# Performance work log

Measured on AMD Instinct MI355X. Metric: run time of the kernel, lower is better.

Reference implementation:

```python
import jax, jax.numpy as jnp
import numpy as np

T, B, D, H = 2048, 2, 1024, 16
DPH = D // H
SCALE = DPH ** -0.5


def setup_inputs() -> dict:
    key = jax.random.key(0)
    ks = jax.random.split(key, 5)
    x = jax.random.normal(ks[0], (T, B, D), dtype=jnp.float32)
    Wk = jax.random.normal(ks[1], (D, D), dtype=jnp.float32) * 0.02
    Wv = jax.random.normal(ks[2], (D, D), dtype=jnp.float32) * 0.02
    Wq = jax.random.normal(ks[3], (D, D), dtype=jnp.float32) * 0.02
    Wo = jax.random.normal(ks[4], (D, D), dtype=jnp.float32) * 0.02
    # causal mask: True marks positions to hide (masked_fill semantics)
    mask = jnp.triu(jnp.ones((T, T), dtype=bool), k=1)
    return {"x": x, "Wk": Wk, "Wv": Wv, "Wq": Wq, "Wo": Wo, "mask": mask}


def _split_heads(y):
    # 't b (d h) -> b h t d' : d_per_head is the OUTER factor of the split
    t, b, _ = y.shape
    return y.reshape(t, b, DPH, H).transpose(1, 3, 0, 2)  # [b, h, t, d]


def reference(x, Wk, Wv, Wq, Wo, mask):
    # nn.Linear(bias=False): y = x @ W.T
    k = _split_heads(x @ Wk.T)
    v = _split_heads(x @ Wv.T)
    q = _split_heads(x @ Wq.T)
    scores = jnp.einsum('bhid,bhjd->bhij', q, k) * SCALE  # [b,h,t,t]
    scores = jnp.where(mask, -jnp.inf, scores)
    attn = jax.nn.softmax(scores, axis=-1)
    # dropout is identity in eval mode
    out = jnp.einsum('bhij,bhjd->bhid', attn, v)  # [b,h,t,d]
    # 'b h t d -> t b (h d)' : heads are the OUTER factor of the merge
    out = out.transpose(2, 0, 1, 3).reshape(x.shape[0], x.shape[1], D)
    return out @ Wo.T
```

## Files before the change

### kernel.cpp

```cpp
#include <hip/hip_runtime.h>

#define T_LEN   2048
#define BATCH   2
#define DMODEL  1024
#define NHEAD   16
#define DHEAD   64
#define MROWS   4096
#define KDIM    1024
#define NDIM    1024
#define ATT_SC2 (0.125f * 1.44269504088896f)

typedef unsigned short u16;
typedef unsigned int   u32;
typedef u16   u16x8 __attribute__((ext_vector_type(8)));
typedef u16   u16x4 __attribute__((ext_vector_type(4)));
typedef u32   u32x4 __attribute__((ext_vector_type(4)));
typedef __bf16 bf16x8 __attribute__((ext_vector_type(8)));
typedef float f32x4  __attribute__((ext_vector_type(4)));
typedef float f32x16 __attribute__((ext_vector_type(16)));

__device__ __forceinline__ u16 f2bf(float f) {
  u32 u = __builtin_bit_cast(u32, f);
  u += 0x7fffu + ((u >> 16) & 1u);
  return (u16)(u >> 16);
}

__device__ __forceinline__ u16 bfc(float f) {
  return __builtin_bit_cast(u16, (__bf16)f);
}

__device__ __forceinline__ f32x4 mfma16(u16x8 a, u16x8 b, f32x4 c) {
  return __builtin_amdgcn_mfma_f32_16x16x32_bf16(
      __builtin_bit_cast(bf16x8, a), __builtin_bit_cast(bf16x8, b), c, 0, 0, 0);
}

__device__ __forceinline__ f32x16 mfma32(u16x8 a, u16x8 b, f32x16 c) {
  return __builtin_amdgcn_mfma_f32_32x32x16_bf16(
      __builtin_bit_cast(bf16x8, a), __builtin_bit_cast(bf16x8, b), c, 0, 0, 0);
}

__device__ __forceinline__ f32x16 mfma32p(u32x4 a, u16x8 b, f32x16 c) {
  return __builtin_amdgcn_mfma_f32_32x32x16_bf16(
      __builtin_bit_cast(bf16x8, a), __builtin_bit_cast(bf16x8, b), c, 0, 0, 0);
}

__device__ __forceinline__ u32 cvtpk(float lo, float hi) {
  u32 r;
  asm("v_cvt_pk_bf16_f32 %0, %1, %2" : "=v"(r) : "v"(lo), "v"(hi));
  return r;
}

__device__ __forceinline__ void pswap(u32& a, u32& b) {
  asm volatile("v_permlane32_swap_b32 %0, %1" : "+v"(a), "+v"(b));
}

__device__ __forceinline__ void gload16(const u16* g, u16* l) {
  __builtin_amdgcn_global_load_lds((const __attribute__((address_space(1))) void*)g,
                                   (__attribute__((address_space(3))) void*)l,
                                   16, 0, 0);
}

#define XN 4194304u
__global__ __launch_bounds__(256) void cast_all(
    const float* __restrict__ x,  const float* __restrict__ wk,
    const float* __restrict__ wv, const float* __restrict__ wq,
    const float* __restrict__ wo, u16* __restrict__ ws) {
  size_t i = ((size_t)blockIdx.x * 256 + threadIdx.x) * 4;
  const float* src; size_t soff, doff; float sc = 1.0f;
  if (i < XN) {
    int m = (int)(i >> 10), d = (int)(i & 1023);
    int t = m >> 1, b = m & 1;
    src = x; soff = i;
    doff = ((size_t)(b * 2048 + t) << 10) + d;
  } else {
    size_t off = i - XN;
    int wi = (int)(off >> 20);
    off &= 1048575u;
    int u = (int)(off >> 10), c = (int)(off & 1023);
    src = (wi == 0) ? wk : (wi == 1) ? wv : (wi == 2) ? wq : wo;
    soff = off;
    if (wi == 3) {
      doff = XN + 3u * 1048576u + off;
    } else {
      int slot = (wi == 2) ? 0 : (wi == 0) ? 1 : 2;
      int up = (u & 15) * 64 + (u >> 4);
      doff = XN + (size_t)slot * 1048576u + ((size_t)up << 10) + c;
      if (wi == 2) sc = ATT_SC2;
    }
  }
  float4 v = *reinterpret_cast<const float4*>(src + soff);
  u16x4 o;
  o.s0 = f2bf(v.x * sc); o.s1 = f2bf(v.y * sc); o.s2 = f2bf(v.z * sc); o.s3 = f2bf(v.w * sc);
  *reinterpret_cast<u16x4*>(ws + doff) = o;
}

__global__ __launch_bounds__(256, 2) void gemm_qkv(
    const u16* __restrict__ xbm, const u16* __restrict__ Wqkv,
    u16* __restrict__ Qh, u16* __restrict__ Kh, u16* __restrict__ Vt) {
  __shared__ __align__(16) u16 As[256 * 64];
  __shared__ __align__(16) u16 Bs[128 * 64];

  const int tid = threadIdx.x;
  const int l  = tid & 63, w = tid >> 6;
  const int lr = l & 15,  lg = l >> 4;
  const int wm = w >> 1,  wn = w & 1;

  const int blk  = blockIdx.x;
  const int wgid = (blk & 7) * 48 + (blk >> 3);

  const u16 *A, *W;
  int m0, n0, isV;
  if (wgid < 256) {
    const int bx = wgid >> 4, by = wgid & 15;
    A = xbm; W = Wqkv; m0 = by * 256; n0 = bx * 128; isV = 0;
  } else {
    const int v = wgid - 256;
    const int vby = v >> 5, vbx = v & 31;
    A = Wqkv + (2048u << 10); W = xbm; m0 = vby * 256; n0 = vbx * 128; isV = 1;
  }

  f32x4 acc[8][4];
#pragma unroll
  for (int i = 0; i < 8; ++i)
#pragma unroll
    for (int j = 0; j < 4; ++j) acc[i][j] = (f32x4)(0.0f);

  for (int k0 = 0; k0 < KDIM; k0 += 64) {
#pragma unroll
    for (int i = 0; i < 8; ++i) {
      const int base = i * 256 + w * 64;
      const int p = base + l;
      const int r = p >> 3, c = p & 7;
      gload16(A + (size_t)(m0 + r) * KDIM + k0 + ((c ^ (r & 7)) << 3),
              As + (size_t)base * 8);
    }
#pragma unroll
    for (int i = 0; i < 4; ++i) {
      const int base = i * 256 + w * 64;
      const int p = base + l;
      const int r = p >> 3, c = p & 7;
      gload16(W + (size_t)(n0 + r) * KDIM + k0 + ((c ^ (r & 7)) << 3),
              Bs + (size_t)base * 8);
    }
    __syncthreads();

#pragma unroll
    for (int ks = 0; ks < 2; ++ks) {
      const int cr = ks * 4 + lg;
      u16x8 bf_[4];
#pragma unroll
      for (int ni = 0; ni < 4; ++ni) {
        const int rr = wn * 64 + ni * 16 + lr;
        bf_[ni] = *reinterpret_cast<const u16x8*>(Bs + rr * 64 + ((cr ^ (rr & 7)) << 3));
      }
      __builtin_amdgcn_s_setprio(1);
#pragma unroll
      for (int mi = 0; mi < 8; ++mi) {
        const int rr = wm * 128 + mi * 16 + lr;
        const u16x8 af = *reinterpret_cast<const u16x8*>(
            As + rr * 64 + ((cr ^ (rr & 7)) << 3));
#pragma unroll
        for (int ni = 0; ni < 4; ++ni)
          acc[mi][ni] = mfma16(af, bf_[ni], acc[mi][ni]);
      }
      __builtin_amdgcn_s_setprio(0);
    }
    __syncthreads();
  }

#pragma unroll
  for (int mi = 0; mi < 8; ++mi)
#pragma unroll
    for (int ni = 0; ni < 4; ++ni)
#pragma unroll
      for (int r = 0; r < 4; ++r) {
        const int row = m0 + wm * 128 + mi * 16 + lg * 4 + r;
        const int col = n0 + wn * 64 + ni * 16 + lr;
        const u16 v = bfc(acc[mi][ni][r]);
        if (!isV) {
          const int bb = row >> 11, t = row & 2047;
          const int c = col & 1023, hh = c >> 6, dp = c & 63;
          u16* d = (col < 1024) ? Qh : Kh;
          d[(((size_t)(bb * NHEAD + hh) << 11) + t) * 64 + dp] = v;
        } else {
          const int hh = row >> 6, dp = row & 63;
          const int bb = col >> 11, t = col & 2047;
          Vt[((((size_t)(bb * NHEAD + hh)) * 64 + dp) << 11) + t] = v;
        }
      }
}

__global__ __launch_bounds__(256) void gemm_o(
    const u16* __restrict__ A, const u16* __restrict__ W, float* __restrict__ out) {
  __shared__ __align__(16) u16 As[128 * 64];
  __shared__ __align__(16) u16 Bs[64 * 64];

  const int tid = threadIdx.x;
  const int l  = tid & 63, w = tid >> 6;
  const int lr = l & 15,  lg = l >> 4;
  const int wm = w >> 1,  wn = w & 1;

  const int blk  = blockIdx.x;
  const int wgid = (blk & 7) * 64 + (blk >> 3);
  const int bx = wgid >> 5, by = wgid & 31;
  const int m0 = by * 128;
  const int n0 = bx * 64;

  f32x4 acc[4][2];
#pragma unroll
  for (int i = 0; i < 4; ++i)
#pragma unroll
    for (int j = 0; j < 2; ++j) acc[i][j] = (f32x4)(0.0f);

  for (int k0 = 0; k0 < KDIM; k0 += 64) {
#pragma unroll
    for (int i = 0; i < 4; ++i) {
      const int base = i * 256 + w * 64;
      const int p = base + l;
      const int r = p >> 3, c = p & 7;
      gload16(A + (size_t)(m0 + r) * KDIM + k0 + ((c ^ (r & 7)) << 3),
              As + (size_t)base * 8);
    }
#pragma unroll
    for (int i = 0; i < 2; ++i) {
      const int base = i * 256 + w * 64;
      const int p = base + l;
      const int r = p >> 3, c = p & 7;
      gload16(W + (size_t)(n0 + r) * KDIM + k0 + ((c ^ (r & 7)) << 3),
              Bs + (size_t)base * 8);
    }
    __syncthreads();

#pragma unroll
    for (int ks = 0; ks < 2; ++ks) {
      const int cr = ks * 4 + lg;
      u16x8 bf_[2];
#pragma unroll
      for (int ni = 0; ni < 2; ++ni) {
        const int rr = wn * 32 + ni * 16 + lr;
        bf_[ni] = *reinterpret_cast<const u16x8*>(Bs + rr * 64 + ((cr ^ (rr & 7)) << 3));
      }
      __builtin_amdgcn_s_setprio(1);
#pragma unroll
      for (int mi = 0; mi < 4; ++mi) {
        const int rr = wm * 64 + mi * 16 + lr;
        const u16x8 af = *reinterpret_cast<const u16x8*>(
            As + rr * 64 + ((cr ^ (rr & 7)) << 3));
#pragma unroll
        for (int ni = 0; ni < 2; ++ni)
          acc[mi][ni] = mfma16(af, bf_[ni], acc[mi][ni]);
      }
      __builtin_amdgcn_s_setprio(0);
    }
    __syncthreads();
  }

#pragma unroll
  for (int mi = 0; mi < 4; ++mi)
#pragma unroll
    for (int ni = 0; ni < 2; ++ni)
#pragma unroll
      for (int r = 0; r < 4; ++r) {
        const int row = m0 + wm * 64 + mi * 16 + lg * 4 + r;
        const int col = n0 + wn * 32 + ni * 16 + lr;
        const int t = row & 2047, bb = row >> 11;
        out[((size_t)(t * 2 + bb) << 10) + col] = acc[mi][ni][r];
      }
}

__global__ __launch_bounds__(256, 2) void attn_fwd(
    const u16* __restrict__ Qh, const u16* __restrict__ Kh,
    const u16* __restrict__ Vt, u16* __restrict__ Aout) {
  __shared__ __align__(16) u16 smem[32768];

  const int tid = threadIdx.x;
  const int l = tid & 63, w = tid >> 6;
  const int l31 = l & 31, hi = l >> 5;
  const int wk = w & 1, wq = w >> 1;
  const int blk = blockIdx.x;
  const int bxx = (blk >> 3) & 15;
  const int bh  = ((blk >> 7) << 3) + (blk & 7);
  const int b = bh >> 4, h = bh & 15;

  const u16* kg = Kh + ((size_t)bh << 17);
  const u16* vg = Vt + ((size_t)bh << 17);

  float* redO = reinterpret_cast<float*>(smem);
  float* redS = redO + 4352;

  auto stage = [&](int buf, int kv0) {
    u16* kb = smem + buf * 8192;
    u16* vb = smem + 16384 + buf * 8192;
#pragma unroll
    for (int j = 0; j < 4; ++j) {
      const int base = (j * 4 + w) * 64;
      const int gg = base + l;
      const int rk = gg >> 3, ck = gg & 7;
      gload16(kg + (size_t)(kv0 + rk) * 64 + ((ck ^ (rk & 7)) << 3),
              kb + (size_t)base * 8);
      const int rv = gg >> 4, cv = gg & 15;
      gload16(vg + ((size_t)rv << 11) + kv0 + ((cv ^ (rv & 15)) << 3),
              vb + (size_t)base * 8);
    }
  };

  for (int ph = 0; ph < 2; ++ph) {
    const int qb = ph ? bxx : 31 - bxx;
    const int qbw = qb * 64 + wq * 32;
    const int q31 = qbw + l31;

    const u16* qptr = Qh + (((size_t)bh << 11) + q31) * 64 + hi * 8;
    u16x8 qf[4];
#pragma unroll
    for (int ks = 0; ks < 4; ++ks)
      qf[ks] = *reinterpret_cast<const u16x8*>(qptr + ks * 16);

    f32x16 acc0 = (f32x16)(0.0f), acc1 = (f32x16)(0.0f);
    float sumw = 0.0f;

    const int npair = (qb + 2) >> 1;
    stage(0, 0);
    __syncthreads();

    int cur = 0;
    for (int t = 0; t < npair; ++t) {
      const int kv0 = t * 128;
      const bool pf = (t + 1 < npair);
      if (pf) {
        stage(cur ^ 1, kv0 + 128);
        asm volatile("s_waitcnt vmcnt(8)" ::: "memory");
      } else {
        asm volatile("s_waitcnt vmcnt(0)" ::: "memory");
      }
      __builtin_amdgcn_sched_barrier(0);
      __builtin_amdgcn_s_barrier();

      const int kvw = kv0 + wk * 64;
      if (kvw <= qbw + 31) {
        const u16* kb = smem + cur * 8192;
        const u16* vb = smem + 16384 + cur * 8192;

#pragma unroll
        for (int tile = 0; tile < 2; ++tile) {
          const int tb = kvw + tile * 32;
          if (tb <= qbw + 31) {
            f32x16 s16 = (f32x16)(0.0f);
            __builtin_amdgcn_s_setprio(1);
#pragma unroll
            for (int ks = 0; ks < 4; ++ks) {
              const int row = wk * 64 + tile * 32 + l31;
              const u16x8 kf = *reinterpret_cast<const u16x8*>(
                  kb + row * 64 + (((2 * ks + hi) ^ (row & 7)) << 3));
              s16 = mfma32(kf, qf[ks], s16);
            }
            __builtin_amdgcn_s_setprio(0);

            const bool diag = (tb + 31 > qbw);
#pragma unroll
            for (int i = 0; i < 16; ++i) {
              float s = s16[i];
              if (diag) {
                const int kv = tb + (i & 3) + 8 * (i >> 2) + 4 * hi;
                if (kv > q31) s = -1e30f;
              }
              s16[i] = __builtin_amdgcn_exp2f(s - 8.0f);
            }
            float ts = 0.0f;
#pragma unroll
            for (int i = 0; i < 16; ++i) ts += s16[i];
            sumw += ts;

#pragma unroll
            for (int ks2 = 0; ks2 < 2; ++ks2) {
              const int pb = ks2 * 8;
              u32 a0 = cvtpk(s16[pb + 0], s16[pb + 1]);
              u32 b0 = cvtpk(s16[pb + 4], s16[pb + 5]);
              u32 a1 = cvtpk(s16[pb + 2], s16[pb + 3]);
              u32 b1 = cvtpk(s16[pb + 6], s16[pb + 7]);
              pswap(a0, b0);
              pswap(a1, b1);
              u32x4 pa;
              pa.x = a0; pa.y = a1; pa.z = b0; pa.w = b1;

              const int cc = wk * 8 + tile * 4 + ks2 * 2 + hi;
              __builtin_amdgcn_s_setprio(1);
              {
                const int dr0 = l31;
                const u16x8 vf0 = *reinterpret_cast<const u16x8*>(
                    vb + dr0 * 128 + ((cc ^ (dr0 & 15)) << 3));
                acc0 = mfma32p(pa, vf0, acc0);
                const int dr1 = 32 + l31;
                const u16x8 vf1 = *reinterpret_cast<const u16x8*>(
                    vb + dr1 * 128 + ((cc ^ (dr1 & 15)) << 3));
                acc1 = mfma32p(pa, vf1, acc1);
              }
              __builtin_amdgcn_s_setprio(0);
            }
          }
        }
      }

      asm volatile("s_waitcnt lgkmcnt(0)" ::: "memory");
      __builtin_amdgcn_sched_barrier(0);
      __builtin_amdgcn_s_barrier();
      cur ^= 1;
    }

    const float sfull = sumw + __shfl_xor(sumw, 32, 64);

    if (wk) {
      float* po = redO + wq * 2176;
#pragma unroll
      for (int i = 0; i < 16; ++i) {
        const int qr = (i & 3) + 8 * (i >> 2) + 4 * hi;
        po[qr * 68 + l31]      = acc0[i];
        po[qr * 68 + 32 + l31] = acc1[i];
      }
      if (l < 32) redS[wq * 32 + l] = sfull;
    }
    __syncthreads();

    if (!wk) {
      const float* po = redO + wq * 2176;
      const float ssT  = sfull + redS[wq * 32 + l31];
      const float invL = 1.0f / ssT;
#pragma unroll
      for (int i = 0; i < 16; ++i) {
        const int qr = (i & 3) + 8 * (i >> 2) + 4 * hi;
        const float inv = __shfl(invL, qr, 64);
        const int q = qbw + qr;
        const size_t rb = (((size_t)(b * 2048 + q)) << 10) + h * DHEAD;
        Aout[rb + l31]      = bfc((acc0[i] + po[qr * 68 + l31]) * inv);
        Aout[rb + 32 + l31] = bfc((acc1[i] + po[qr * 68 + 32 + l31]) * inv);
      }
    }
    __syncthreads();
  }
}

extern "C" void kernel_launch(void* const* d_in, const int* in_sizes, int n_in,
                              void* d_out, int out_size, void* d_ws, size_t ws_size,
                              hipStream_t stream) {
  const float* x  = (const float*)d_in[0];
  const float* Wk = (const float*)d_in[1];
  const float* Wv = (const float*)d_in[2];
  const float* Wq = (const float*)d_in[3];
  const float* Wo = (const float*)d_in[4];

  u16* ws   = (u16*)d_ws;
  u16* xbm  = ws;
  u16* Wqkv = xbm + 4194304;
  u16* Wob  = Wqkv + 3145728;
  u16* Qh   = Wob + 1048576;
  u16* Kh   = Qh  + 4194304;
  u16* Vt   = Kh  + 4194304;
  u16* Aout = Vt  + 4194304;

  cast_all<<<8192, 256, 0, stream>>>(x, Wk, Wv, Wq, Wo, ws);

  gemm_qkv<<<384, 256, 0, stream>>>(xbm, Wqkv, Qh, Kh, Vt);

  attn_fwd<<<512, 256, 0, stream>>>(Qh, Kh, Vt, Aout);

  gemm_o<<<512, 256, 0, stream>>>(Aout, Wob, (float*)d_out);
}
```

Before: 107.9 us.

## Split attention KV tiles across four waves per query group with 512-thread blocks

Doubles the attention block from 256 to 512 threads. Each query group now uses four waves, each handling one 32-row KV tile per 128-row stage, where before two waves each handled two tiles. The K/V staging loop is halved per wave, and the partial outputs and row sums of three waves are reduced through shared memory into the fourth. This aims to raise parallelism and shorten the per-wave serial loop. In exchange it adds a larger cross-wave reduction, and the tighter launch bound (512 threads, 4 blocks) may limit registers and cause spills.

```diff
diff --git a/kernel.cpp b/kernel.cpp
--- a/kernel.cpp
+++ b/kernel.cpp
@@ -268,7 +268,7 @@
       }
 }
 
-__global__ __launch_bounds__(256, 2) void attn_fwd(
+__global__ __launch_bounds__(512, 4) void attn_fwd(
     const u16* __restrict__ Qh, const u16* __restrict__ Kh,
     const u16* __restrict__ Vt, u16* __restrict__ Aout) {
   __shared__ __align__(16) u16 smem[32768];
@@ -276,7 +276,7 @@
   const int tid = threadIdx.x;
   const int l = tid & 63, w = tid >> 6;
   const int l31 = l & 31, hi = l >> 5;
-  const int wk = w & 1, wq = w >> 1;
+  const int wk = w & 3, wq = w >> 2;
   const int blk = blockIdx.x;
   const int bxx = (blk >> 3) & 15;
   const int bh  = ((blk >> 7) << 3) + (blk & 7);
@@ -286,14 +286,14 @@
   const u16* vg = Vt + ((size_t)bh << 17);
 
   float* redO = reinterpret_cast<float*>(smem);
-  float* redS = redO + 4352;
+  float* redS = redO + 13056;
 
   auto stage = [&](int buf, int kv0) {
     u16* kb = smem + buf * 8192;
     u16* vb = smem + 16384 + buf * 8192;
 #pragma unroll
-    for (int j = 0; j < 4; ++j) {
-      const int base = (j * 4 + w) * 64;
+    for (int j = 0; j < 2; ++j) {
+      const int base = (j * 8 + w) * 64;
       const int gg = base + l;
       const int rk = gg >> 3, ck = gg & 7;
       gload16(kg + (size_t)(kv0 + rk) * 64 + ((ck ^ (rk & 7)) << 3),
@@ -328,75 +328,69 @@
       const bool pf = (t + 1 < npair);
       if (pf) {
         stage(cur ^ 1, kv0 + 128);
-        asm volatile("s_waitcnt vmcnt(8)" ::: "memory");
+        asm volatile("s_waitcnt vmcnt(4)" ::: "memory");
       } else {
         asm volatile("s_waitcnt vmcnt(0)" ::: "memory");
       }
       __builtin_amdgcn_sched_barrier(0);
       __builtin_amdgcn_s_barrier();
 
-      const int kvw = kv0 + wk * 64;
+      const int kvw = kv0 + wk * 32;
       if (kvw <= qbw + 31) {
         const u16* kb = smem + cur * 8192;
         const u16* vb = smem + 16384 + cur * 8192;
 
-#pragma unroll
-        for (int tile = 0; tile < 2; ++tile) {
-          const int tb = kvw + tile * 32;
-          if (tb <= qbw + 31) {
-            f32x16 s16 = (f32x16)(0.0f);
-            __builtin_amdgcn_s_setprio(1);
-#pragma unroll
-            for (int ks = 0; ks < 4; ++ks) {
-              const int row = wk * 64 + tile * 32 + l31;
-              const u16x8 kf = *reinterpret_cast<const u16x8*>(
-                  kb + row * 64 + (((2 * ks + hi) ^ (row & 7)) << 3));
-              s16 = mfma32(kf, qf[ks], s16);
-            }
-            __builtin_amdgcn_s_setprio(0);
-
-            const bool diag = (tb + 31 > qbw);
-#pragma unroll
-            for (int i = 0; i < 16; ++i) {
-              float s = s16[i];
-              if (diag) {
-                const int kv = tb + (i & 3) + 8 * (i >> 2) + 4 * hi;
-                if (kv > q31) s = -1e30f;
-              }
-              s16[i] = __builtin_amdgcn_exp2f(s - 8.0f);
-            }
-            float ts = 0.0f;
-#pragma unroll
-            for (int i = 0; i < 16; ++i) ts += s16[i];
-            sumw += ts;
-
-#pragma unroll
-            for (int ks2 = 0; ks2 < 2; ++ks2) {
-              const int pb = ks2 * 8;
-              u32 a0 = cvtpk(s16[pb + 0], s16[pb + 1]);
-              u32 b0 = cvtpk(s16[pb + 4], s16[pb + 5]);
-              u32 a1 = cvtpk(s16[pb + 2], s16[pb + 3]);
-              u32 b1 = cvtpk(s16[pb + 6], s16[pb + 7]);
-              pswap(a0, b0);
-              pswap(a1, b1);
-              u32x4 pa;
-              pa.x = a0; pa.y = a1; pa.z = b0; pa.w = b1;
-
-              const int cc = wk * 8 + tile * 4 + ks2 * 2 + hi;
-              __builtin_amdgcn_s_setprio(1);
-              {
-                const int dr0 = l31;
-                const u16x8 vf0 = *reinterpret_cast<const u16x8*>(
-                    vb + dr0 * 128 + ((cc ^ (dr0 & 15)) << 3));
-                acc0 = mfma32p(pa, vf0, acc0);
-                const int dr1 = 32 + l31;
-                const u16x8 vf1 = *reinterpret_cast<const u16x8*>(
-                    vb + dr1 * 128 + ((cc ^ (dr1 & 15)) << 3));
-                acc1 = mfma32p(pa, vf1, acc1);
-              }
-              __builtin_amdgcn_s_setprio(0);
-            }
+        f32x16 s16 = (f32x16)(0.0f);
+        __builtin_amdgcn_s_setprio(1);
+#pragma unroll
+        for (int ks = 0; ks < 4; ++ks) {
+          const int row = wk * 32 + l31;
+          const u16x8 kf = *reinterpret_cast<const u16x8*>(
+              kb + row * 64 + (((2 * ks + hi) ^ (row & 7)) << 3));
+          s16 = mfma32(kf, qf[ks], s16);
+        }
+        __builtin_amdgcn_s_setprio(0);
+
+        const bool diag = (kvw + 31 > qbw);
+#pragma unroll
+        for (int i = 0; i < 16; ++i) {
+          float s = s16[i];
+          if (diag) {
+            const int kv = kvw + (i & 3) + 8 * (i >> 2) + 4 * hi;
+            if (kv > q31) s = -1e30f;
           }
+          s16[i] = __builtin_amdgcn_exp2f(s - 8.0f);
+        }
+        float ts = 0.0f;
+#pragma unroll
+        for (int i = 0; i < 16; ++i) ts += s16[i];
+        sumw += ts;
+
+#pragma unroll
+        for (int ks2 = 0; ks2 < 2; ++ks2) {
+          const int pb = ks2 * 8;
+          u32 a0 = cvtpk(s16[pb + 0], s16[pb + 1]);
+          u32 b0 = cvtpk(s16[pb + 4], s16[pb + 5]);
+          u32 a1 = cvtpk(s16[pb + 2], s16[pb + 3]);
+          u32 b1 = cvtpk(s16[pb + 6], s16[pb + 7]);
+          pswap(a0, b0);
+          pswap(a1, b1);
+          u32x4 pa;
+          pa.x = a0; pa.y = a1; pa.z = b0; pa.w = b1;
+
+          const int cc = wk * 4 + ks2 * 2 + hi;
+          __builtin_amdgcn_s_setprio(1);
+          {
+            const int dr0 = l31;
+            const u16x8 vf0 = *reinterpret_cast<const u16x8*>(
+                vb + dr0 * 128 + ((cc ^ (dr0 & 15)) << 3));
+            acc0 = mfma32p(pa, vf0, acc0);
+            const int dr1 = 32 + l31;
+            const u16x8 vf1 = *reinterpret_cast<const u16x8*>(
+                vb + dr1 * 128 + ((cc ^ (dr1 & 15)) << 3));
+            acc1 = mfma32p(pa, vf1, acc1);
+          }
+          __builtin_amdgcn_s_setprio(0);
         }
       }
 
@@ -409,29 +403,38 @@
     const float sfull = sumw + __shfl_xor(sumw, 32, 64);
 
     if (wk) {
-      float* po = redO + wq * 2176;
+      float* po = redO + (wq * 3 + wk - 1) * 2176;
 #pragma unroll
       for (int i = 0; i < 16; ++i) {
         const int qr = (i & 3) + 8 * (i >> 2) + 4 * hi;
         po[qr * 68 + l31]      = acc0[i];
         po[qr * 68 + 32 + l31] = acc1[i];
       }
-      if (l < 32) redS[wq * 32 + l] = sfull;
+      if (l < 32) redS[(wq * 3 + wk - 1) * 32 + l] = sfull;
     }
     __syncthreads();
 
     if (!wk) {
-      const float* po = redO + wq * 2176;
-      const float ssT  = sfull + redS[wq * 32 + l31];
-      const float invL = 1.0f / ssT;
+      float ss = sfull;
+#pragma unroll
+      for (int j = 0; j < 3; ++j)
+        ss += redS[(wq * 3 + j) * 32 + l31];
+      const float invL = 1.0f / ss;
 #pragma unroll
       for (int i = 0; i < 16; ++i) {
         const int qr = (i & 3) + 8 * (i >> 2) + 4 * hi;
         const float inv = __shfl(invL, qr, 64);
+        float o0 = acc0[i], o1 = acc1[i];
+#pragma unroll
+        for (int j = 0; j < 3; ++j) {
+          const float* po = redO + (wq * 3 + j) * 2176;
+          o0 += po[qr * 68 + l31];
+          o1 += po[qr * 68 + 32 + l31];
+        }
         const int q = qbw + qr;
         const size_t rb = (((size_t)(b * 2048 + q)) << 10) + h * DHEAD;
-        Aout[rb + l31]      = bfc((acc0[i] + po[qr * 68 + l31]) * inv);
-        Aout[rb + 32 + l31] = bfc((acc1[i] + po[qr * 68 + 32 + l31]) * inv);
+        Aout[rb + l31]      = bfc(o0 * inv);
+        Aout[rb + 32 + l31] = bfc(o1 * inv);
       }
     }
     __syncthreads();
@@ -460,7 +463,7 @@
 
   gemm_qkv<<<384, 256, 0, stream>>>(xbm, Wqkv, Qh, Kh, Vt);
 
-  attn_fwd<<<512, 256, 0, stream>>>(Qh, Kh, Vt, Aout);
+  attn_fwd<<<512, 512, 0, stream>>>(Qh, Kh, Vt, Aout);
 
   gemm_o<<<512, 256, 0, stream>>>(Aout, Wob, (float*)d_out);
 }
```

Measured after the change: 132.3 us. +22.7%, slower.
